# Kernel tuning notes

Measured on AMD Instinct MI355X. Metric: run time of the kernel, lower is better.

Reference implementation:

```python
import jax, jax.numpy as jnp
import numpy as np

T = 4096
HIDDEN = 2048
N_HEADS = 16
N_KV_HEADS = 4
HEAD_DIM = 128
WINDOW = 1024  # per_layer_sliding_window = WINDOW + 1 -> q attends keys with q_pos - k_pos <= WINDOW
ROPE_THETA = 100000.0
QKV_OUT = (N_HEADS + 2 * N_KV_HEADS) * HEAD_DIM  # 3072


def setup_inputs() -> dict:
    key = jax.random.key(0)
    k1, k2, k3, k4 = jax.random.split(key, 4)
    return {
        "hidden_states": jax.random.normal(k1, (T, HIDDEN), dtype=jnp.float32),
        "positions": jnp.arange(T, dtype=jnp.int32),
        "w_qkv": jax.random.normal(k2, (HIDDEN, QKV_OUT), dtype=jnp.float32) * 0.02,
        "b_qkv": jax.random.normal(k3, (QKV_OUT,), dtype=jnp.float32) * 0.02,
        "w_o": jax.random.normal(k4, (N_HEADS * HEAD_DIM, HIDDEN), dtype=jnp.float32) * 0.02,
    }


def _apply_rope(x, positions):
    # x: [T, n_heads, HEAD_DIM], neox-style rotary over full head dim
    half = HEAD_DIM // 2
    inv_freq = 1.0 / (ROPE_THETA ** (jnp.arange(half, dtype=jnp.float32) / half))
    freqs = positions.astype(jnp.float32)[:, None] * inv_freq[None, :]  # [T, half]
    cos = jnp.cos(freqs)[:, None, :]  # [T, 1, half]
    sin = jnp.sin(freqs)[:, None, :]
    x1, x2 = x[..., :half], x[..., half:]
    return jnp.concatenate([x1 * cos - x2 * sin, x2 * cos + x1 * sin], axis=-1)


def reference(hidden_states, positions, w_qkv, b_qkv, w_o):
    # QKV projection (bias=True)
    qkv = hidden_states @ w_qkv + b_qkv  # [T, QKV_OUT]
    q_size = N_HEADS * HEAD_DIM
    kv_size = N_KV_HEADS * HEAD_DIM
    q = qkv[:, :q_size].reshape(T, N_HEADS, HEAD_DIM)
    k = qkv[:, q_size:q_size + kv_size].reshape(T, N_KV_HEADS, HEAD_DIM)
    v = qkv[:, q_size + kv_size:].reshape(T, N_KV_HEADS, HEAD_DIM)

    # RoPE on q and k
    q = _apply_rope(q, positions)
    k = _apply_rope(k, positions)

    # GQA: expand kv heads to match query heads
    group = N_HEADS // N_KV_HEADS
    k = jnp.repeat(k, group, axis=1)  # [T, N_HEADS, HEAD_DIM]
    v = jnp.repeat(v, group, axis=1)

    scale = HEAD_DIM ** -0.5
    scores = jnp.einsum('qhd,khd->hqk', q, k) * scale  # [H, T, T]

    # causal + sliding-window mask: j <= i and i - j <= WINDOW
    i = jnp.arange(T)[:, None]
    j = jnp.arange(T)[None, :]
    mask = (j <= i) & (i - j <= WINDOW)  # [T, T]
    scores = jnp.where(mask[None, :, :], scores, jnp.finfo(scores.dtype).min)

    probs = jax.nn.softmax(scores, axis=-1)
    attn = jnp.einsum('hqk,khd->qhd', probs, v)  # [T, H, HEAD_DIM]
    attn = attn.reshape(T, N_HEADS * HEAD_DIM)

    # output projection (bias=False)
    return attn @ w_o
```

## Files before the change

kernel.cpp:

```cpp
#include <hip/hip_runtime.h>
#include <cstdint>

#define T_TOK 4096
#define HID 2048
#define NH 16
#define NKV 4
#define HD 128
#define WIN 1024
#define QKVO 3072

typedef float f32x4 __attribute__((ext_vector_type(4)));
typedef __bf16 bf16x8 __attribute__((ext_vector_type(8)));
typedef __bf16 bf16x4 __attribute__((ext_vector_type(4)));
typedef __bf16 bf16x2 __attribute__((ext_vector_type(2)));

__device__ __forceinline__ void gload16(const void* g, void* lds) {
  auto gp = reinterpret_cast<__attribute__((address_space(1))) void*>(
      reinterpret_cast<uintptr_t>(g));
  auto lp = reinterpret_cast<__attribute__((address_space(3))) void*>(
      reinterpret_cast<uintptr_t>(lds));
  __builtin_amdgcn_global_load_lds(gp, lp, 16, 0, 0);
}

__device__ __forceinline__ f32x4 mfma16(bf16x8 a, bf16x8 b, f32x4 c) {
  return __builtin_amdgcn_mfma_f32_16x16x32_bf16(a, b, c, 0, 0, 0);
}

__global__ __launch_bounds__(256) void k_f32_to_bf16(const float* __restrict__ x,
                                                     __bf16* __restrict__ y) {
  const size_t e = (size_t)blockIdx.x * 256 + threadIdx.x;
  const float4* xv = (const float4*)x;
  float4 a = xv[e * 2], b = xv[e * 2 + 1];
  bf16x8 o;
  o[0] = (__bf16)a.x; o[1] = (__bf16)a.y; o[2] = (__bf16)a.z; o[3] = (__bf16)a.w;
  o[4] = (__bf16)b.x; o[5] = (__bf16)b.y; o[6] = (__bf16)b.z; o[7] = (__bf16)b.w;
  *(bf16x8*)(y + e * 8) = o;
}

__global__ __launch_bounds__(256) void k_transpose(const float* __restrict__ W,
                                                   __bf16* __restrict__ Wt,
                                                   int R, int C) {
  __shared__ __bf16 tb[32][33];
  const int nbx = C >> 5;
  const int c0 = (blockIdx.x % nbx) << 5;
  const int r0 = (blockIdx.x / nbx) << 5;
  const int tx = threadIdx.x & 31, ty = threadIdx.x >> 5;
#pragma unroll
  for (int i = 0; i < 32; i += 8)
    tb[ty + i][tx] = (__bf16)W[(size_t)(r0 + ty + i) * C + c0 + tx];
  __syncthreads();
#pragma unroll
  for (int i = 0; i < 32; i += 8)
    Wt[(size_t)(c0 + ty + i) * R + r0 + tx] = tb[tx][ty + i];
}

__global__ void k_rope_tab(const int* __restrict__ pos, float* __restrict__ cosT,
                           float* __restrict__ sinT) {
  const int t = blockIdx.x;
  const int d = threadIdx.x;
  const float inv = exp2f(-(float)d * (16.609640474436812f / 64.0f));
  const float fr = (float)pos[t] * inv;
  cosT[t * 64 + d] = cosf(fr);
  sinT[t * 64 + d] = sinf(fr);
}

template <bool BIAS, typename OutT>
__global__ __launch_bounds__(256, 2) void k_gemm(const __bf16* __restrict__ A,
                                                 const __bf16* __restrict__ Bt,
                                                 const float* __restrict__ bias,
                                                 OutT* __restrict__ C,
                                                 int M, int N, int K) {
  __shared__ __align__(16) __bf16 As[2][128 * 32];
  __shared__ __align__(16) __bf16 Bs[2][128 * 32];
  const int tid = threadIdx.x;
  const int lane = tid & 63;
  const int w = tid >> 6;
  const int wr = w >> 1, wc = w & 1;
  const int c = lane & 15, g = lane >> 4;
  const int gsw = g ^ ((c >> 1) & 3);

  const int nstc = N >> 9;
  const int bid = blockIdx.x;
  const int xcd = bid & 7;
  const int j = bid >> 3;
  const int spx = (int)(gridDim.x >> 7);
  const int s = xcd * spx + (j >> 4);
  const int q = j & 15;
  const int by = (s / nstc) * 4 + (q >> 2);
  const int bx = (s % nstc) * 4 + (q & 3);
  const int m0 = by << 7, n0 = bx << 7;

  const int o0 = w * 2048 + lane * 16;
  const int r0 = o0 >> 6;
  const int g0 = (lane & 3) ^ ((r0 >> 1) & 3);
  const int o1 = o0 + 1024;
  const int r1 = o1 >> 6;
  const int g1 = (lane & 3) ^ ((r1 >> 1) & 3);
  const __bf16* gA0 = A + (size_t)(m0 + r0) * K + g0 * 8;
  const __bf16* gA1 = A + (size_t)(m0 + r1) * K + g1 * 8;
  const __bf16* gB0 = Bt + (size_t)(n0 + r0) * K + g0 * 8;
  const __bf16* gB1 = Bt + (size_t)(n0 + r1) * K + g1 * 8;

  f32x4 acc[4][4] = {};

  {
    char* la = (char*)&As[0][0];
    char* lb = (char*)&Bs[0][0];
    gload16(gA0, la + o0);
    gload16(gA1, la + o1);
    gload16(gB0, lb + o0);
    gload16(gB1, lb + o1);
  }
  __syncthreads();

  int cur = 0;
  for (int kt = 0; kt < K; kt += 32) {
    if (kt + 32 < K) {
      char* la = (char*)&As[0][0] + (cur ^ 1) * 8192;
      char* lb = (char*)&Bs[0][0] + (cur ^ 1) * 8192;
      gload16(gA0 + kt + 32, la + o0);
      gload16(gA1 + kt + 32, la + o1);
      gload16(gB0 + kt + 32, lb + o0);
      gload16(gB1 + kt + 32, lb + o1);
    }
    const __bf16* as = &As[0][0] + cur * 4096;
    const __bf16* bs = &Bs[0][0] + cur * 4096;
    bf16x8 af[4], bfr[4];
#pragma unroll
    for (int mi = 0; mi < 4; mi++)
      af[mi] = *(const bf16x8*)(as + (wr * 64 + mi * 16 + c) * 32 + gsw * 8);
#pragma unroll
    for (int ni = 0; ni < 4; ni++)
      bfr[ni] = *(const bf16x8*)(bs + (wc * 64 + ni * 16 + c) * 32 + gsw * 8);
#pragma unroll
    for (int mi = 0; mi < 4; mi++)
#pragma unroll
      for (int ni = 0; ni < 4; ni++)
        acc[mi][ni] = mfma16(af[mi], bfr[ni], acc[mi][ni]);
    __syncthreads();
    cur ^= 1;
  }

#pragma unroll
  for (int ni = 0; ni < 4; ni++) {
    const int col = n0 + wc * 64 + ni * 16 + c;
    const float bv = BIAS ? bias[col] : 0.0f;
#pragma unroll
    for (int mi = 0; mi < 4; mi++)
#pragma unroll
      for (int r = 0; r < 4; r++) {
        const int row = m0 + wr * 64 + mi * 16 + 4 * g + r;
        C[(size_t)row * N + col] = (OutT)(acc[mi][ni][r] + bv);
      }
  }
}

__global__ __launch_bounds__(256) void k_rope_pack(
    const __bf16* __restrict__ qkv, const float* __restrict__ cosT,
    const float* __restrict__ sinT, __bf16* __restrict__ Qp,
    __bf16* __restrict__ Kp, __bf16* __restrict__ Vt) {
  const int t0 = blockIdx.x * 64;
  const int hh = blockIdx.y;
  const int tid = threadIdx.x;
  const int col0 = hh * HD;
  __shared__ __bf16 lt[64][136];
  if (hh < NH + NKV) {
    const bool isq = hh < NH;
    const float s = isq ? (0.08838834764831845f * 1.4426950408889634f) : 1.0f;
    __bf16* base = isq ? (Qp + (size_t)hh * T_TOK * HD)
                       : (Kp + (size_t)(hh - NH) * T_TOK * HD);
#pragma unroll
    for (int jj = 0; jj < 2; jj++) {
      const int e = jj * 256 + tid;
      const int tl = e >> 3, ch = e & 7;
      const int tt = t0 + tl;
      const bf16x8 x1 = *(const bf16x8*)(qkv + (size_t)tt * QKVO + col0 + ch * 8);
      const bf16x8 x2 = *(const bf16x8*)(qkv + (size_t)tt * QKVO + col0 + 64 + ch * 8);
      const float4 c0 = *(const float4*)(cosT + tt * 64 + ch * 8);
      const float4 c1 = *(const float4*)(cosT + tt * 64 + ch * 8 + 4);
      const float4 s0 = *(const float4*)(sinT + tt * 64 + ch * 8);
      const float4 s1 = *(const float4*)(sinT + tt * 64 + ch * 8 + 4);
      const float cs[8] = {c0.x, c0.y, c0.z, c0.w, c1.x, c1.y, c1.z, c1.w};
      const float sn[8] = {s0.x, s0.y, s0.z, s0.w, s1.x, s1.y, s1.z, s1.w};
      bf16x8 o1, o2;
#pragma unroll
      for (int i = 0; i < 8; i++) {
        const float a = (float)x1[i], b = (float)x2[i];
        o1[i] = (__bf16)((a * cs[i] - b * sn[i]) * s);
        o2[i] = (__bf16)((b * cs[i] + a * sn[i]) * s);
      }
      const int d2s = isq ? ch * 8 : ((ch * 8) ^ ((tt & 7) << 3));
      __bf16* dst = base + (size_t)tt * HD;
      *(bf16x8*)(dst + d2s) = o1;
      *(bf16x8*)(dst + 64 + d2s) = o2;
    }
  } else {
    const int kv = hh - (NH + NKV);
#pragma unroll
    for (int jj = 0; jj < 4; jj++) {
      const int e = jj * 256 + tid;
      const int tl = e >> 4, dc = e & 15;
      *(bf16x8*)&lt[tl][dc * 8] =
          *(const bf16x8*)(qkv + (size_t)(t0 + tl) * QKVO + col0 + dc * 8);
    }
    __syncthreads();
#pragma unroll
    for (int jj = 0; jj < 32; jj++) {
      const int e = jj * 256 + tid;
      const int d = e >> 6, tl = e & 63;
      Vt[((size_t)kv * HD + d) * T_TOK + t0 + (tl ^ ((d & 7) << 3))] = lt[tl][d];
    }
  }
}

__global__ __launch_bounds__(256, 2) void k_attn(const __bf16* __restrict__ Qp,
                                                 const __bf16* __restrict__ Kp,
                                                 const __bf16* __restrict__ Vt,
                                                 __bf16* __restrict__ attnO) {
  __shared__ __align__(16) __bf16 Ks[2][64 * 128];
  __shared__ __align__(16) __bf16 Vs[2][128 * 64];
  __shared__ __align__(16) __bf16 Ps[4][32 * 64];

  const int tid = threadIdx.x;
  const int lane = tid & 63;
  const int w = tid >> 6;
  const int c = lane & 15, g = lane >> 4;
  const int h = blockIdx.y;
  const int kvh = h >> 2;
  const int qb = (int)(gridDim.x - 1) - (int)blockIdx.x;
  const int q0 = qb * 128;
  const int iw = q0 + 32 * w;
  const int swz = (c & 7) << 4;

  bf16x8 qf[2][4];
#pragma unroll
  for (int qh = 0; qh < 2; qh++) {
    const __bf16* qbase = Qp + ((size_t)h * T_TOK + iw + 16 * qh + c) * HD;
#pragma unroll
    for (int ds = 0; ds < 4; ds++)
      qf[qh][ds] = *(const bf16x8*)(qbase + ds * 32 + g * 8);
  }

  f32x4 ot[2][8] = {};
  float mrun[2] = {0.0f, 0.0f}, lrun[2] = {0.0f, 0.0f};

  const int jstart = (q0 >= WIN) ? (q0 - WIN) : 0;
  const int niter = (q0 + 128 - jstart) >> 6;

  const char* Kg = (const char*)Kp + (size_t)kvh * T_TOK * HD * 2;
  const char* Vg = (const char*)Vt + (size_t)kvh * HD * T_TOK * 2;
  const char* kg0 = Kg + (size_t)(jstart + 16 * w + (lane >> 4)) * 256 + (lane & 15) * 16;
  const char* vg0 = Vg + (size_t)(32 * w + (lane >> 3)) * (T_TOK * 2) +
                    (size_t)jstart * 2 + (lane & 7) * 16;

#pragma unroll
  for (int q = 0; q < 4; q++)
    gload16(kg0 + q * 1024, (char*)&Ks[0][0] + w * 4096 + q * 1024);
#pragma unroll
  for (int q = 0; q < 4; q++)
    gload16(vg0 + (size_t)q * 8 * (T_TOK * 2), (char*)&Vs[0][0] + w * 4096 + q * 1024);

  char* pw = (char*)&Ps[w][0];
  int cur = 0;

  for (int it = 0; it < niter; ++it) {
    const int j0 = jstart + it * 64;
    __syncthreads();

    if (it + 1 < niter) {
      const char* kg = kg0 + (size_t)(it + 1) * 16384;
      const char* vg = vg0 + (size_t)(it + 1) * 128;
      char* kd = (char*)&Ks[cur ^ 1][0] + w * 4096;
      char* vd = (char*)&Vs[cur ^ 1][0] + w * 4096;
#pragma unroll
      for (int q = 0; q < 4; q++) gload16(kg + q * 1024, kd + q * 1024);
#pragma unroll
      for (int q = 0; q < 4; q++)
        gload16(vg + (size_t)q * 8 * (T_TOK * 2), vd + q * 1024);
    }

    const char* kb = (const char*)&Ks[cur][0];
    const char* vb = (const char*)&Vs[cur][0];

    f32x4 st[2][4] = {};
    __builtin_amdgcn_s_setprio(1);
#pragma unroll
    for (int t = 0; t < 4; t++)
#pragma unroll
      for (int ds = 0; ds < 4; ds++) {
        bf16x8 kf = *(const bf16x8*)(kb + (t * 16 + c) * 256 + ((ds * 64 + g * 16) ^ swz));
        st[0][t] = mfma16(kf, qf[0][ds], st[0][t]);
        st[1][t] = mfma16(kf, qf[1][ds], st[1][t]);
      }
    __builtin_amdgcn_s_setprio(0);

#pragma unroll
    for (int qh = 0; qh < 2; qh++) {
      const int rlo = iw + 16 * qh;
      const int irow = rlo + c;
      float p[16];
      float cmax = -1e30f;
      if ((j0 + 63 <= rlo) && (rlo + 15 - j0 <= WIN)) {
#pragma unroll
        for (int t = 0; t < 4; t++)
#pragma unroll
          for (int r = 0; r < 4; r++) {
            const float s = st[qh][t][r];
            p[t * 4 + r] = s;
            cmax = fmaxf(cmax, s);
          }
      } else {
        const int jb = irow - j0 - 4 * g;
#pragma unroll
        for (int t = 0; t < 4; t++)
#pragma unroll
          for (int r = 0; r < 4; r++) {
            float s = st[qh][t][r];
            s = ((unsigned)(jb - 16 * t - r) <= WIN) ? s : -1e30f;
            p[t * 4 + r] = s;
            cmax = fmaxf(cmax, s);
          }
      }
      cmax = fmaxf(cmax, __shfl_xor(cmax, 16));
      cmax = fmaxf(cmax, __shfl_xor(cmax, 32));

      if (!__all(cmax <= mrun[qh] + 11.54f)) {
        const float mn = fmaxf(mrun[qh], cmax);
        const float alpha = exp2f(mrun[qh] - mn);
        lrun[qh] *= alpha;
#pragma unroll
        for (int m = 0; m < 8; m++) ot[qh][m] *= alpha;
        mrun[qh] = mn;
      }
      float rs = 0.0f;
#pragma unroll
      for (int x = 0; x < 16; x++) {
        const float e_ = exp2f(p[x] - mrun[qh]);
        p[x] = e_;
        rs += e_;
      }
      rs += __shfl_xor(rs, 16);
      rs += __shfl_xor(rs, 32);
      lrun[qh] += rs;

#pragma unroll
      for (int t = 0; t < 4; t++) {
        bf16x4 pk;
        pk[0] = (__bf16)p[t * 4 + 0];
        pk[1] = (__bf16)p[t * 4 + 1];
        pk[2] = (__bf16)p[t * 4 + 2];
        pk[3] = (__bf16)p[t * 4 + 3];
        *(bf16x4*)(pw + (16 * qh + c) * 128 + ((t * 32 + g * 8) ^ swz)) = pk;
      }
    }

    bf16x8 pf[2][2];
#pragma unroll
    for (int qh = 0; qh < 2; qh++)
#pragma unroll
      for (int ks = 0; ks < 2; ks++)
        pf[qh][ks] =
            *(const bf16x8*)(pw + (16 * qh + c) * 128 + ((ks * 64 + g * 16) ^ swz));

    __builtin_amdgcn_s_setprio(1);
#pragma unroll
    for (int m = 0; m < 8; m++)
#pragma unroll
      for (int ks = 0; ks < 2; ks++) {
        bf16x8 vf = *(const bf16x8*)(vb + (m * 16 + c) * 128 + ((ks * 64 + g * 16) ^ swz));
        ot[0][m] = mfma16(vf, pf[0][ks], ot[0][m]);
        ot[1][m] = mfma16(vf, pf[1][ks], ot[1][m]);
      }
    __builtin_amdgcn_s_setprio(0);

    cur ^= 1;
  }

#pragma unroll
  for (int qh = 0; qh < 2; qh++) {
    const float inv_l = 1.0f / lrun[qh];
    __bf16* orow = attnO + (size_t)(iw + 16 * qh + c) * (NH * HD) + h * HD;
#pragma unroll
    for (int m = 0; m < 8; m++) {
      bf16x4 o4;
#pragma unroll
      for (int r = 0; r < 4; r++) o4[r] = (__bf16)(ot[qh][m][r] * inv_l);
      *(bf16x4*)(orow + m * 16 + 4 * g) = o4;
    }
  }
}

extern "C" void kernel_launch(void* const* d_in, const int* in_sizes, int n_in,
                              void* d_out, int out_size, void* d_ws, size_t ws_size,
                              hipStream_t stream) {
  (void)in_sizes; (void)n_in; (void)out_size; (void)ws_size;
  const float* hidden = (const float*)d_in[0];
  const int* positions = (const int*)d_in[1];
  const float* w_qkv = (const float*)d_in[2];
  const float* b_qkv = (const float*)d_in[3];
  const float* w_o = (const float*)d_in[4];
  float* out = (float*)d_out;

  char* ws = (char*)d_ws;
  __bf16* Hb = (__bf16*)ws;    ws += (size_t)T_TOK * HID * 2;
  __bf16* Wqkvt = (__bf16*)ws; ws += (size_t)QKVO * HID * 2;
  __bf16* Wot = (__bf16*)ws;   ws += (size_t)HID * HID * 2;
  float* cosT = (float*)ws;    ws += (size_t)T_TOK * 64 * 4;
  float* sinT = (float*)ws;    ws += (size_t)T_TOK * 64 * 4;
  __bf16* qkv = (__bf16*)ws;   ws += (size_t)T_TOK * QKVO * 2;
  __bf16* Qp = (__bf16*)ws;    ws += (size_t)NH * T_TOK * HD * 2;
  __bf16* Kp = (__bf16*)ws;    ws += (size_t)NKV * T_TOK * HD * 2;
  __bf16* Vt = (__bf16*)ws;    ws += (size_t)NKV * HD * T_TOK * 2;
  __bf16* attnb = (__bf16*)ws; ws += (size_t)T_TOK * NH * HD * 2;

  k_f32_to_bf16<<<T_TOK * HID / (256 * 8), 256, 0, stream>>>(hidden, Hb);
  k_transpose<<<(QKVO / 32) * (HID / 32), 256, 0, stream>>>(w_qkv, Wqkvt, HID, QKVO);
  k_transpose<<<(HID / 32) * (HID / 32), 256, 0, stream>>>(w_o, Wot, HID, HID);
  k_rope_tab<<<T_TOK, 64, 0, stream>>>(positions, cosT, sinT);
  k_gemm<true, __bf16><<<(T_TOK / 128) * (QKVO / 128), 256, 0, stream>>>(
      Hb, Wqkvt, b_qkv, qkv, T_TOK, QKVO, HID);
  k_rope_pack<<<dim3(T_TOK / 64, NH + 2 * NKV), 256, 0, stream>>>(
      qkv, cosT, sinT, Qp, Kp, Vt);
  k_attn<<<dim3(T_TOK / 128, NH), 256, 0, stream>>>(Qp, Kp, Vt, attnb);
  k_gemm<false, float><<<(T_TOK / 128) * (HID / 128), 256, 0, stream>>>(
      attnb, Wot, nullptr, out, T_TOK, HID, HID);
}
```

Measured before the change: 194.8 us.

## Switch attention to 32x32x16 MFMA with register-resident P via permlane swap

Rewrites the attention inner loop to use 32x32x16 bf16 MFMA tiles, one 32-row query tile per wave instead of two 16-row halves. The softmax probabilities are packed with v_cvt_pk_bf16_f32 and rearranged with v_permlane32_swap into B-operand layout, so the per-wave LDS round trip for P and its buffer are removed. It also adds per-wave skipping of KV tiles that lie entirely outside the causal or sliding window. The costs are heavier accumulator register use and reliance on gfx950-specific instructions.

```diff
diff --git a/kernel.cpp b/kernel.cpp
--- a/kernel.cpp
+++ b/kernel.cpp
@@ -10,9 +10,10 @@
 #define QKVO 3072
 
 typedef float f32x4 __attribute__((ext_vector_type(4)));
+typedef float f32x16 __attribute__((ext_vector_type(16)));
 typedef __bf16 bf16x8 __attribute__((ext_vector_type(8)));
 typedef __bf16 bf16x4 __attribute__((ext_vector_type(4)));
-typedef __bf16 bf16x2 __attribute__((ext_vector_type(2)));
+typedef unsigned int u32x4 __attribute__((ext_vector_type(4)));
 
 __device__ __forceinline__ void gload16(const void* g, void* lds) {
   auto gp = reinterpret_cast<__attribute__((address_space(1))) void*>(
@@ -24,6 +25,17 @@
 
 __device__ __forceinline__ f32x4 mfma16(bf16x8 a, bf16x8 b, f32x4 c) {
   return __builtin_amdgcn_mfma_f32_16x16x32_bf16(a, b, c, 0, 0, 0);
+}
+__device__ __forceinline__ f32x16 mfma32(bf16x8 a, bf16x8 b, f32x16 c) {
+  return __builtin_amdgcn_mfma_f32_32x32x16_bf16(a, b, c, 0, 0, 0);
+}
+__device__ __forceinline__ unsigned cvtpk(float lo, float hi) {
+  unsigned r;
+  asm("v_cvt_pk_bf16_f32 %0, %1, %2" : "=v"(r) : "v"(lo), "v"(hi));
+  return r;
+}
+__device__ __forceinline__ void pl32swap(unsigned& a, unsigned& b) {
+  asm volatile("v_permlane32_swap_b32 %0, %1" : "+v"(a), "+v"(b));
 }
 
 __global__ __launch_bounds__(256) void k_f32_to_bf16(const float* __restrict__ x,
@@ -219,30 +231,30 @@
                                                  __bf16* __restrict__ attnO) {
   __shared__ __align__(16) __bf16 Ks[2][64 * 128];
   __shared__ __align__(16) __bf16 Vs[2][128 * 64];
-  __shared__ __align__(16) __bf16 Ps[4][32 * 64];
 
   const int tid = threadIdx.x;
   const int lane = tid & 63;
   const int w = tid >> 6;
-  const int c = lane & 15, g = lane >> 4;
+  const int l31 = lane & 31;
+  const int hi = lane >> 5;
+  const int swz = (lane & 7) << 4;
   const int h = blockIdx.y;
   const int kvh = h >> 2;
   const int qb = (int)(gridDim.x - 1) - (int)blockIdx.x;
   const int q0 = qb * 128;
   const int iw = q0 + 32 * w;
-  const int swz = (c & 7) << 4;
-
-  bf16x8 qf[2][4];
-#pragma unroll
-  for (int qh = 0; qh < 2; qh++) {
-    const __bf16* qbase = Qp + ((size_t)h * T_TOK + iw + 16 * qh + c) * HD;
-#pragma unroll
-    for (int ds = 0; ds < 4; ds++)
-      qf[qh][ds] = *(const bf16x8*)(qbase + ds * 32 + g * 8);
-  }
-
-  f32x4 ot[2][8] = {};
-  float mrun[2] = {0.0f, 0.0f}, lrun[2] = {0.0f, 0.0f};
+  const int irow = iw + l31;
+
+  bf16x8 qf[8];
+  {
+    const __bf16* qbase = Qp + ((size_t)h * T_TOK + irow) * HD;
+#pragma unroll
+    for (int ds = 0; ds < 8; ds++)
+      qf[ds] = *(const bf16x8*)(qbase + ds * 16 + hi * 8);
+  }
+
+  f32x16 ot[4] = {};
+  float mrun = 0.0f, lrun = 0.0f;
 
   const int jstart = (q0 >= WIN) ? (q0 - WIN) : 0;
   const int niter = (q0 + 128 - jstart) >> 6;
@@ -260,7 +272,6 @@
   for (int q = 0; q < 4; q++)
     gload16(vg0 + (size_t)q * 8 * (T_TOK * 2), (char*)&Vs[0][0] + w * 4096 + q * 1024);
 
-  char* pw = (char*)&Ps[w][0];
   int cur = 0;
 
   for (int it = 0; it < niter; ++it) {
@@ -279,115 +290,114 @@
         gload16(vg + (size_t)q * 8 * (T_TOK * 2), vd + q * 1024);
     }
 
+    if (j0 > iw + 31) { cur ^= 1; continue; }
+    if (iw - (j0 + 63) > WIN) { cur ^= 1; continue; }
+
     const char* kb = (const char*)&Ks[cur][0];
     const char* vb = (const char*)&Vs[cur][0];
 
-    f32x4 st[2][4] = {};
+    f32x16 st[2] = {};
     __builtin_amdgcn_s_setprio(1);
 #pragma unroll
-    for (int t = 0; t < 4; t++)
-#pragma unroll
-      for (int ds = 0; ds < 4; ds++) {
-        bf16x8 kf = *(const bf16x8*)(kb + (t * 16 + c) * 256 + ((ds * 64 + g * 16) ^ swz));
-        st[0][t] = mfma16(kf, qf[0][ds], st[0][t]);
-        st[1][t] = mfma16(kf, qf[1][ds], st[1][t]);
+    for (int t = 0; t < 2; t++)
+#pragma unroll
+      for (int ds = 0; ds < 8; ds++) {
+        bf16x8 kf = *(const bf16x8*)(kb + (t * 32 + l31) * 256 +
+                                     ((ds * 32 + hi * 16) ^ swz));
+        st[t] = mfma32(kf, qf[ds], st[t]);
       }
     __builtin_amdgcn_s_setprio(0);
 
-#pragma unroll
-    for (int qh = 0; qh < 2; qh++) {
-      const int rlo = iw + 16 * qh;
-      const int irow = rlo + c;
-      float p[16];
-      float cmax = -1e30f;
-      if ((j0 + 63 <= rlo) && (rlo + 15 - j0 <= WIN)) {
-#pragma unroll
-        for (int t = 0; t < 4; t++)
-#pragma unroll
-          for (int r = 0; r < 4; r++) {
-            const float s = st[qh][t][r];
-            p[t * 4 + r] = s;
-            cmax = fmaxf(cmax, s);
-          }
-      } else {
-        const int jb = irow - j0 - 4 * g;
-#pragma unroll
-        for (int t = 0; t < 4; t++)
-#pragma unroll
-          for (int r = 0; r < 4; r++) {
-            float s = st[qh][t][r];
-            s = ((unsigned)(jb - 16 * t - r) <= WIN) ? s : -1e30f;
-            p[t * 4 + r] = s;
-            cmax = fmaxf(cmax, s);
-          }
-      }
-      cmax = fmaxf(cmax, __shfl_xor(cmax, 16));
-      cmax = fmaxf(cmax, __shfl_xor(cmax, 32));
-
-      if (!__all(cmax <= mrun[qh] + 11.54f)) {
-        const float mn = fmaxf(mrun[qh], cmax);
-        const float alpha = exp2f(mrun[qh] - mn);
-        lrun[qh] *= alpha;
-#pragma unroll
-        for (int m = 0; m < 8; m++) ot[qh][m] *= alpha;
-        mrun[qh] = mn;
-      }
-      float rs = 0.0f;
-#pragma unroll
-      for (int x = 0; x < 16; x++) {
-        const float e_ = exp2f(p[x] - mrun[qh]);
-        p[x] = e_;
+    float p[2][16];
+    float cmax = -1e30f;
+    const bool interior = (j0 + 63 <= iw) && (iw + 31 - j0 <= WIN);
+    if (interior) {
+#pragma unroll
+      for (int t = 0; t < 2; t++)
+#pragma unroll
+        for (int r = 0; r < 16; r++) {
+          const float s = st[t][r];
+          p[t][r] = s;
+          cmax = fmaxf(cmax, s);
+        }
+    } else {
+      const int jb = irow - j0 - 4 * hi;
+#pragma unroll
+      for (int t = 0; t < 2; t++)
+#pragma unroll
+        for (int r = 0; r < 16; r++) {
+          float s = st[t][r];
+          const int off = 32 * t + (r & 3) + 8 * (r >> 2);
+          s = ((unsigned)(jb - off) <= WIN) ? s : -1e30f;
+          p[t][r] = s;
+          cmax = fmaxf(cmax, s);
+        }
+    }
+    cmax = fmaxf(cmax, __shfl_xor(cmax, 32));
+
+    if (!__all(cmax <= mrun + 11.54f)) {
+      const float mn = fmaxf(mrun, cmax);
+      const float alpha = exp2f(mrun - mn);
+      lrun *= alpha;
+#pragma unroll
+      for (int m = 0; m < 4; m++) ot[m] *= alpha;
+      mrun = mn;
+    }
+    float rs = 0.0f;
+#pragma unroll
+    for (int t = 0; t < 2; t++)
+#pragma unroll
+      for (int r = 0; r < 16; r++) {
+        const float e_ = exp2f(p[t][r] - mrun);
+        p[t][r] = e_;
         rs += e_;
       }
-      rs += __shfl_xor(rs, 16);
-      rs += __shfl_xor(rs, 32);
-      lrun[qh] += rs;
-
-#pragma unroll
-      for (int t = 0; t < 4; t++) {
-        bf16x4 pk;
-        pk[0] = (__bf16)p[t * 4 + 0];
-        pk[1] = (__bf16)p[t * 4 + 1];
-        pk[2] = (__bf16)p[t * 4 + 2];
-        pk[3] = (__bf16)p[t * 4 + 3];
-        *(bf16x4*)(pw + (16 * qh + c) * 128 + ((t * 32 + g * 8) ^ swz)) = pk;
+    rs += __shfl_xor(rs, 32);
+    lrun += rs;
+
+    bf16x8 pb[4];
+#pragma unroll
+    for (int t = 0; t < 2; t++) {
+      unsigned wds[8];
+#pragma unroll
+      for (int i = 0; i < 8; i++) wds[i] = cvtpk(p[t][2 * i], p[t][2 * i + 1]);
+      pl32swap(wds[0], wds[2]);
+      pl32swap(wds[1], wds[3]);
+      pl32swap(wds[4], wds[6]);
+      pl32swap(wds[5], wds[7]);
+      u32x4 f0 = {wds[0], wds[1], wds[2], wds[3]};
+      u32x4 f1 = {wds[4], wds[5], wds[6], wds[7]};
+      pb[2 * t] = __builtin_bit_cast(bf16x8, f0);
+      pb[2 * t + 1] = __builtin_bit_cast(bf16x8, f1);
+    }
+
+    __builtin_amdgcn_s_setprio(1);
+#pragma unroll
+    for (int m = 0; m < 4; m++) {
+      const char* vrow = vb + (m * 32 + l31) * 128;
+#pragma unroll
+      for (int ks = 0; ks < 4; ks++) {
+        bf16x8 vf = *(const bf16x8*)(vrow + ((ks * 32 + hi * 16) ^ swz));
+        ot[m] = mfma32(vf, pb[ks], ot[m]);
       }
     }
-
-    bf16x8 pf[2][2];
-#pragma unroll
-    for (int qh = 0; qh < 2; qh++)
-#pragma unroll
-      for (int ks = 0; ks < 2; ks++)
-        pf[qh][ks] =
-            *(const bf16x8*)(pw + (16 * qh + c) * 128 + ((ks * 64 + g * 16) ^ swz));
-
-    __builtin_amdgcn_s_setprio(1);
-#pragma unroll
-    for (int m = 0; m < 8; m++)
-#pragma unroll
-      for (int ks = 0; ks < 2; ks++) {
-        bf16x8 vf = *(const bf16x8*)(vb + (m * 16 + c) * 128 + ((ks * 64 + g * 16) ^ swz));
-        ot[0][m] = mfma16(vf, pf[0][ks], ot[0][m]);
-        ot[1][m] = mfma16(vf, pf[1][ks], ot[1][m]);
-      }
     __builtin_amdgcn_s_setprio(0);
 
     cur ^= 1;
   }
 
-#pragma unroll
-  for (int qh = 0; qh < 2; qh++) {
-    const float inv_l = 1.0f / lrun[qh];
-    __bf16* orow = attnO + (size_t)(iw + 16 * qh + c) * (NH * HD) + h * HD;
-#pragma unroll
-    for (int m = 0; m < 8; m++) {
+  const float inv_l = 1.0f / lrun;
+  __bf16* orow = attnO + (size_t)irow * (NH * HD) + h * HD;
+#pragma unroll
+  for (int m = 0; m < 4; m++)
+#pragma unroll
+    for (int rg = 0; rg < 4; rg++) {
+      const int d0 = 32 * m + 8 * rg + 4 * hi;
       bf16x4 o4;
 #pragma unroll
-      for (int r = 0; r < 4; r++) o4[r] = (__bf16)(ot[qh][m][r] * inv_l);
-      *(bf16x4*)(orow + m * 16 + 4 * g) = o4;
-    }
-  }
+      for (int r = 0; r < 4; r++) o4[r] = (__bf16)(ot[m][4 * rg + r] * inv_l);
+      *(bf16x4*)(orow + d0) = o4;
+    }
 }
 
 extern "C" void kernel_launch(void* const* d_in, const int* in_sizes, int n_in,
```

Result: faster. 189.2 us (-2.9%).
